# Optimization experiments

Measured on AMD Instinct MI355X. Metric: run time of the kernel, lower is better.

The kernel has to match this reference:

```python
import jax, jax.numpy as jnp
import numpy as np

N_NODES = 50000
N_EDGES = 1600000
NODE_DIM = 64
EDGE_DIM = 64
HID = 64
EPS = 1e-5


def _linear(x, W, b):
    return x @ W + b


def _layernorm(x, g, b):
    m = jnp.mean(x, axis=-1, keepdims=True)
    v = jnp.mean((x - m) ** 2, axis=-1, keepdims=True)
    return (x - m) * jax.lax.rsqrt(v + EPS) * g + b


def _mlp(x, p, pre):
    # Linear-ReLU, Linear-ReLU, Linear-LayerNorm
    h = jax.nn.relu(_linear(x, p[pre + 'W1'], p[pre + 'b1']))
    h = jax.nn.relu(_linear(h, p[pre + 'W2'], p[pre + 'b2']))
    h = _linear(h, p[pre + 'W3'], p[pre + 'b3'])
    return _layernorm(h, p[pre + 'g'], p[pre + 'beta'])


def setup_inputs() -> dict:
    key = jax.random.key(0)
    ks = jax.random.split(key, 16)
    inp = {
        'node_feat': jax.random.normal(ks[0], (N_NODES, NODE_DIM), jnp.float32),
        'edge_feat': jax.random.normal(ks[1], (N_EDGES, EDGE_DIM), jnp.float32),
        'edge_idx': jax.random.randint(ks[2], (N_EDGES, 2), 0, N_NODES, jnp.int32),
        'node_size': N_NODES,
    }
    s = 0.05
    e_in = EDGE_DIM + 2 * NODE_DIM
    n_in = NODE_DIM + EDGE_DIM
    inp['eW1'] = jax.random.normal(ks[3], (e_in, HID), jnp.float32) * s
    inp['eb1'] = jnp.zeros((HID,), jnp.float32)
    inp['eW2'] = jax.random.normal(ks[4], (HID, HID), jnp.float32) * s
    inp['eb2'] = jnp.zeros((HID,), jnp.float32)
    inp['eW3'] = jax.random.normal(ks[5], (HID, HID), jnp.float32) * s
    inp['eb3'] = jnp.zeros((HID,), jnp.float32)
    inp['eg'] = jnp.ones((HID,), jnp.float32)
    inp['ebeta'] = jnp.zeros((HID,), jnp.float32)
    inp['nW1'] = jax.random.normal(ks[6], (n_in, HID), jnp.float32) * s
    inp['nb1'] = jnp.zeros((HID,), jnp.float32)
    inp['nW2'] = jax.random.normal(ks[7], (HID, HID), jnp.float32) * s
    inp['nb2'] = jnp.zeros((HID,), jnp.float32)
    inp['nW3'] = jax.random.normal(ks[8], (HID, HID), jnp.float32) * s
    inp['nb3'] = jnp.zeros((HID,), jnp.float32)
    inp['ng'] = jnp.ones((HID,), jnp.float32)
    inp['nbeta'] = jnp.zeros((HID,), jnp.float32)
    return inp


def reference(node_feat, edge_feat, edge_idx, node_size,
              eW1, eb1, eW2, eb2, eW3, eb3, eg, ebeta,
              nW1, nb1, nW2, nb2, nW3, nb3, ng, nbeta):
    p = dict(eW1=eW1, eb1=eb1, eW2=eW2, eb2=eb2, eW3=eW3, eb3=eb3, eg=eg, ebeta=ebeta,
             nW1=nW1, nb1=nb1, nW2=nW2, nb2=nb2, nW3=nW3, nb3=nb3, ng=ng, nbeta=nbeta)
    center = edge_idx[:, 0]
    source = edge_idx[:, 1]
    # [E, edge_dim + 2*node_dim]
    stacked = jnp.concatenate([edge_feat, node_feat[center], node_feat[source]], axis=1)
    proc_edge_feat = _mlp(stacked, p, 'e')  # [E, 64]
    # scatter-add aggregate to nodes
    nodal_edge_feat = jax.ops.segment_sum(proc_edge_feat, center, num_segments=node_size)
    stacked_node = jnp.concatenate([node_feat, nodal_edge_feat], axis=1)  # [N, node_dim+64]
    proc_node_feat = _mlp(stacked_node, p, 'n')  # [N, 64]
    return proc_edge_feat, proc_node_feat
```

## Files before the change

kernel.cpp:

```cpp
#include <hip/hip_runtime.h>

typedef unsigned short u16;
typedef unsigned int u32;
typedef __attribute__((ext_vector_type(8))) __bf16 bf16x8;
typedef __attribute__((ext_vector_type(4))) float f32x4;
typedef __attribute__((ext_vector_type(2))) u32 u32x2;
typedef __attribute__((ext_vector_type(4))) u32 u32x4;

__device__ __forceinline__ u16 f2bf(float f) {
    u32 u = __float_as_uint(f);
    u = (u + 0x7FFFu + ((u >> 16) & 1u)) >> 16;
    return (u16)u;
}

__device__ __forceinline__ bf16x8 load8f_bf(const float* p) {
    f32x4 f0 = *(const f32x4*)p;
    f32x4 f1 = *(const f32x4*)(p + 4);
    bf16x8 r;
    r[0] = (__bf16)f0[0]; r[1] = (__bf16)f0[1]; r[2] = (__bf16)f0[2]; r[3] = (__bf16)f0[3];
    r[4] = (__bf16)f1[0]; r[5] = (__bf16)f1[1]; r[6] = (__bf16)f1[2]; r[7] = (__bf16)f1[3];
    return r;
}
__device__ __forceinline__ bf16x8 cvt2bf(f32x4 lo, f32x4 hi) {
    bf16x8 r;
    r[0] = (__bf16)lo[0]; r[1] = (__bf16)lo[1]; r[2] = (__bf16)lo[2]; r[3] = (__bf16)lo[3];
    r[4] = (__bf16)hi[0]; r[5] = (__bf16)hi[1]; r[6] = (__bf16)hi[2]; r[7] = (__bf16)hi[3];
    return r;
}
__device__ __forceinline__ u32 pk2(float x, float y) {
    __bf16 bx = (__bf16)x, by = (__bf16)y;
    return (u32)__builtin_bit_cast(u16, bx) | ((u32)__builtin_bit_cast(u16, by) << 16);
}

#define PK_EW1 0
#define PK_EW2 12288
#define PK_EW3 16384
#define PK_NW1 20480
#define PK_NW2 28672
#define PK_NW3 32768
#define PK_TOTAL 36864

__global__ void pack_weights_kernel(const float* __restrict__ eW1, const float* __restrict__ eW2,
                                    const float* __restrict__ eW3, const float* __restrict__ nW1,
                                    const float* __restrict__ nW2, const float* __restrict__ nW3,
                                    u16* __restrict__ P) {
    int idx = blockIdx.x * blockDim.x + threadIdx.x;
    if (idx >= PK_TOTAL) return;
    const float* W; int base;
    if (idx < PK_EW2)      { W = eW1; base = PK_EW1; }
    else if (idx < PK_EW3) { W = eW2; base = PK_EW2; }
    else if (idx < PK_NW1) { W = eW3; base = PK_EW3; }
    else if (idx < PK_NW2) { W = nW1; base = PK_NW1; }
    else if (idx < PK_NW3) { W = nW2; base = PK_NW2; }
    else                   { W = nW3; base = PK_NW3; }
    int r = idx - base;
    int j = r & 7, lane = (r >> 3) & 63, m = (r >> 9) & 3, s = r >> 11;
    int k = s * 32 + (lane >> 4) * 8 + j;
    int col = 16 * m + (lane & 15);
    P[idx] = f2bf(W[k * 64 + col]);
}

__global__ void degree_kernel(const int* __restrict__ edge_idx, int* __restrict__ deg, int E) {
    int e = blockIdx.x * blockDim.x + threadIdx.x;
    if (e < E) atomicAdd(&deg[edge_idx[2 * e]], 1);
}

__global__ void scan_blocks_kernel(const int* __restrict__ deg, int* __restrict__ off,
                                   int* __restrict__ partials, int N) {
    __shared__ int sh[256];
    const int t = threadIdx.x;
    const int g = blockIdx.x * 256 + t;
    int v = (g < N) ? deg[g] : 0;
    sh[t] = v;
    __syncthreads();
#pragma unroll
    for (int d = 1; d < 256; d <<= 1) {
        int add = (t >= d) ? sh[t - d] : 0;
        __syncthreads();
        sh[t] += add;
        __syncthreads();
    }
    if (g < N) off[g] = sh[t] - v;
    if (t == 255) partials[blockIdx.x] = sh[255];
}

__global__ void scan_partials_kernel(int* __restrict__ partials, int nparts) {
    __shared__ int sh[256];
    const int t = threadIdx.x;
    int v = (t < nparts) ? partials[t] : 0;
    sh[t] = v;
    __syncthreads();
#pragma unroll
    for (int d = 1; d < 256; d <<= 1) {
        int add = (t >= d) ? sh[t - d] : 0;
        __syncthreads();
        sh[t] += add;
        __syncthreads();
    }
    if (t < nparts) partials[t] = sh[t] - v;
}

__global__ void finalize_offsets_kernel(int* __restrict__ off, int* __restrict__ pos,
                                        const int* __restrict__ partials, int N, int E) {
    int g = blockIdx.x * blockDim.x + threadIdx.x;
    if (g < N) {
        int o = off[g] + partials[g >> 8];
        off[g] = o;
        pos[g] = o;
    }
    if (g == 0) off[N] = E;
}

__global__ void fill_csr_kernel(const int* __restrict__ edge_idx, int* __restrict__ pos,
                                int* __restrict__ csr, int E) {
    int e = blockIdx.x * blockDim.x + threadIdx.x;
    if (e < E) {
        int slot = atomicAdd(&pos[edge_idx[2 * e]], 1);
        csr[slot] = e;
    }
}

#define ET 2
__global__ __launch_bounds__(256) void edge_mlp_kernel(
    const float* __restrict__ node_feat, const float* __restrict__ edge_feat,
    const int* __restrict__ edge_idx, const u16* __restrict__ Pw,
    const float* __restrict__ b1g, const float* __restrict__ b2g, const float* __restrict__ b3g,
    const float* __restrict__ gg, const float* __restrict__ betag,
    float* __restrict__ out_edge, int E)
{
    __shared__ float params[5][64];
    __shared__ u16 htile[4][1024];
    const int tid = threadIdx.x;
    if (tid < 64) {
        params[0][tid] = b1g[tid];
        params[1][tid] = b2g[tid];
        params[2][tid] = b3g[tid];
        params[3][tid] = gg[tid];
        params[4][tid] = betag[tid];
    }
    __syncthreads();
    const int wid = tid >> 6, lane = tid & 63;
    const int er = lane & 15, a = lane >> 4;
    const int ebase = (blockIdx.x * 4 + wid) * (16 * ET);
    if (ebase >= E) return;
    u16* ht = htile[wid];
    const int swz = (er & 7) << 4;

    int eidx[ET], cn[ET], sn[ET];
#pragma unroll
    for (int t = 0; t < ET; ++t) {
        int e = ebase + t * 16 + er;
        if (e > E - 1) e = E - 1;
        eidx[t] = e;
        int2 ii = *(const int2*)(edge_idx + 2 * e);
        cn[t] = ii.x; sn[t] = ii.y;
    }

    f32x4 acc[ET][4];
#pragma unroll
    for (int t = 0; t < ET; ++t)
#pragma unroll
        for (int m = 0; m < 4; ++m) acc[t][m] = 0.0f;

#pragma unroll
    for (int s = 0; s < 6; ++s) {
        bf16x8 af[4];
#pragma unroll
        for (int m = 0; m < 4; ++m)
            af[m] = *(const bf16x8*)(Pw + PK_EW1 + ((s * 4 + m) * 64 + lane) * 8);
        bf16x8 bf[ET];
#pragma unroll
        for (int t = 0; t < ET; ++t) {
            const float* src;
            if (s < 2)      src = edge_feat + (size_t)eidx[t] * 64 + s * 32 + a * 8;
            else if (s < 4) src = node_feat + (size_t)cn[t] * 64 + (s - 2) * 32 + a * 8;
            else            src = node_feat + (size_t)sn[t] * 64 + (s - 4) * 32 + a * 8;
            bf[t] = load8f_bf(src);
        }
#pragma unroll
        for (int t = 0; t < ET; ++t)
#pragma unroll
            for (int m = 0; m < 4; ++m)
                acc[t][m] = __builtin_amdgcn_mfma_f32_16x16x32_bf16(af[m], bf[t], acc[t][m], 0, 0, 0);
    }

#pragma unroll
    for (int t = 0; t < ET; ++t) {
#pragma unroll
        for (int m = 0; m < 4; ++m) {
            float v0 = fmaxf(acc[t][m][0] + params[0][16 * m + 4 * a + 0], 0.0f);
            float v1 = fmaxf(acc[t][m][1] + params[0][16 * m + 4 * a + 1], 0.0f);
            float v2 = fmaxf(acc[t][m][2] + params[0][16 * m + 4 * a + 2], 0.0f);
            float v3 = fmaxf(acc[t][m][3] + params[0][16 * m + 4 * a + 3], 0.0f);
            u32x2 pv; pv[0] = pk2(v0, v1); pv[1] = pk2(v2, v3);
            int boff = (er * 128 + (16 * m + 4 * a) * 2) ^ swz;
            *(u32x2*)((char*)ht + boff) = pv;
        }
        f32x4 a2[4];
#pragma unroll
        for (int m = 0; m < 4; ++m) a2[m] = 0.0f;
#pragma unroll
        for (int s = 0; s < 2; ++s) {
            bf16x8 af[4];
#pragma unroll
            for (int m = 0; m < 4; ++m)
                af[m] = *(const bf16x8*)(Pw + PK_EW2 + ((s * 4 + m) * 64 + lane) * 8);
            int boff = (er * 128 + s * 64 + a * 16) ^ swz;
            bf16x8 bf = *(const bf16x8*)((char*)ht + boff);
#pragma unroll
            for (int m = 0; m < 4; ++m)
                a2[m] = __builtin_amdgcn_mfma_f32_16x16x32_bf16(af[m], bf, a2[m], 0, 0, 0);
        }
#pragma unroll
        for (int m = 0; m < 4; ++m) {
            float v0 = fmaxf(a2[m][0] + params[1][16 * m + 4 * a + 0], 0.0f);
            float v1 = fmaxf(a2[m][1] + params[1][16 * m + 4 * a + 1], 0.0f);
            float v2 = fmaxf(a2[m][2] + params[1][16 * m + 4 * a + 2], 0.0f);
            float v3 = fmaxf(a2[m][3] + params[1][16 * m + 4 * a + 3], 0.0f);
            u32x2 pv; pv[0] = pk2(v0, v1); pv[1] = pk2(v2, v3);
            int boff = (er * 128 + (16 * m + 4 * a) * 2) ^ swz;
            *(u32x2*)((char*)ht + boff) = pv;
        }
        f32x4 a3[4];
#pragma unroll
        for (int m = 0; m < 4; ++m) a3[m] = 0.0f;
#pragma unroll
        for (int s = 0; s < 2; ++s) {
            bf16x8 af[4];
#pragma unroll
            for (int m = 0; m < 4; ++m)
                af[m] = *(const bf16x8*)(Pw + PK_EW3 + ((s * 4 + m) * 64 + lane) * 8);
            int boff = (er * 128 + s * 64 + a * 16) ^ swz;
            bf16x8 bf = *(const bf16x8*)((char*)ht + boff);
#pragma unroll
            for (int m = 0; m < 4; ++m)
                a3[m] = __builtin_amdgcn_mfma_f32_16x16x32_bf16(af[m], bf, a3[m], 0, 0, 0);
        }
        float vals[16], sum = 0.0f, ssq = 0.0f;
#pragma unroll
        for (int m = 0; m < 4; ++m)
#pragma unroll
            for (int r = 0; r < 4; ++r) {
                float v = a3[m][r] + params[2][16 * m + 4 * a + r];
                vals[4 * m + r] = v; sum += v; ssq += v * v;
            }
        sum += __shfl_xor(sum, 16, 64); sum += __shfl_xor(sum, 32, 64);
        ssq += __shfl_xor(ssq, 16, 64); ssq += __shfl_xor(ssq, 32, 64);
        const float mean = sum * 0.015625f;
        const float var = ssq * 0.015625f - mean * mean;
        const float inv = rsqrtf(var + 1e-5f);
        const int e = ebase + t * 16 + er;
        if (e < E) {
#pragma unroll
            for (int m = 0; m < 4; ++m) {
                f32x4 o;
#pragma unroll
                for (int r = 0; r < 4; ++r) {
                    int f = 16 * m + 4 * a + r;
                    o[r] = (vals[4 * m + r] - mean) * inv * params[3][f] + params[4][f];
                }
                *(f32x4*)(out_edge + (size_t)e * 64 + 16 * m + 4 * a) = o;
            }
        }
    }
}

__global__ __launch_bounds__(256) void node_mlp_kernel(
    const float* __restrict__ node_feat, const float* __restrict__ proc_edge,
    const int* __restrict__ off, const int* __restrict__ csr,
    const u16* __restrict__ Pw,
    const float* __restrict__ b1g, const float* __restrict__ b2g, const float* __restrict__ b3g,
    const float* __restrict__ gg, const float* __restrict__ betag,
    float* __restrict__ out_node, int N)
{
    __shared__ float params[5][64];
    __shared__ u16 htile[4][1024];
    const int tid = threadIdx.x;
    if (tid < 64) {
        params[0][tid] = b1g[tid];
        params[1][tid] = b2g[tid];
        params[2][tid] = b3g[tid];
        params[3][tid] = gg[tid];
        params[4][tid] = betag[tid];
    }
    __syncthreads();
    const int wid = tid >> 6, lane = tid & 63;
    const int er = lane & 15, a = lane >> 4;
    const int nbase = (blockIdx.x * 4 + wid) * 16;
    if (nbase >= N) return;
    const int n = nbase + er;
    u16* ht = htile[wid];
    const int swz = (er & 7) << 4;

    f32x4 g0a = 0.0f, g0b = 0.0f, g1a = 0.0f, g1b = 0.0f;
    {
        const int beg = off[n], end = off[n + 1];
        int j = beg;
        for (; j + 7 < end; j += 8) {
#pragma unroll
            for (int u = 0; u < 8; ++u) {
                const float* row = proc_edge + (size_t)csr[j + u] * 64;
                g0a += *(const f32x4*)(row + a * 8);
                g0b += *(const f32x4*)(row + a * 8 + 4);
                g1a += *(const f32x4*)(row + 32 + a * 8);
                g1b += *(const f32x4*)(row + 32 + a * 8 + 4);
            }
        }
        for (; j < end; ++j) {
            const float* row = proc_edge + (size_t)csr[j] * 64;
            g0a += *(const f32x4*)(row + a * 8);
            g0b += *(const f32x4*)(row + a * 8 + 4);
            g1a += *(const f32x4*)(row + 32 + a * 8);
            g1b += *(const f32x4*)(row + 32 + a * 8 + 4);
        }
    }

    f32x4 acc[4];
#pragma unroll
    for (int m = 0; m < 4; ++m) acc[m] = 0.0f;

#pragma unroll
    for (int s = 0; s < 4; ++s) {
        bf16x8 af[4];
#pragma unroll
        for (int m = 0; m < 4; ++m)
            af[m] = *(const bf16x8*)(Pw + PK_NW1 + ((s * 4 + m) * 64 + lane) * 8);
        bf16x8 bf;
        if (s < 2)       bf = load8f_bf(node_feat + (size_t)n * 64 + s * 32 + a * 8);
        else if (s == 2) bf = cvt2bf(g0a, g0b);
        else             bf = cvt2bf(g1a, g1b);
#pragma unroll
        for (int m = 0; m < 4; ++m)
            acc[m] = __builtin_amdgcn_mfma_f32_16x16x32_bf16(af[m], bf, acc[m], 0, 0, 0);
    }
#pragma unroll
    for (int m = 0; m < 4; ++m) {
        float v0 = fmaxf(acc[m][0] + params[0][16 * m + 4 * a + 0], 0.0f);
        float v1 = fmaxf(acc[m][1] + params[0][16 * m + 4 * a + 1], 0.0f);
        float v2 = fmaxf(acc[m][2] + params[0][16 * m + 4 * a + 2], 0.0f);
        float v3 = fmaxf(acc[m][3] + params[0][16 * m + 4 * a + 3], 0.0f);
        u32x2 pv; pv[0] = pk2(v0, v1); pv[1] = pk2(v2, v3);
        int boff = (er * 128 + (16 * m + 4 * a) * 2) ^ swz;
        *(u32x2*)((char*)ht + boff) = pv;
    }

#pragma unroll
    for (int m = 0; m < 4; ++m) acc[m] = 0.0f;
#pragma unroll
    for (int s = 0; s < 2; ++s) {
        bf16x8 af[4];
#pragma unroll
        for (int m = 0; m < 4; ++m)
            af[m] = *(const bf16x8*)(Pw + PK_NW2 + ((s * 4 + m) * 64 + lane) * 8);
        int boff = (er * 128 + s * 64 + a * 16) ^ swz;
        bf16x8 bf = *(const bf16x8*)((char*)ht + boff);
#pragma unroll
        for (int m = 0; m < 4; ++m)
            acc[m] = __builtin_amdgcn_mfma_f32_16x16x32_bf16(af[m], bf, acc[m], 0, 0, 0);
    }
#pragma unroll
    for (int m = 0; m < 4; ++m) {
        float v0 = fmaxf(acc[m][0] + params[1][16 * m + 4 * a + 0], 0.0f);
        float v1 = fmaxf(acc[m][1] + params[1][16 * m + 4 * a + 1], 0.0f);
        float v2 = fmaxf(acc[m][2] + params[1][16 * m + 4 * a + 2], 0.0f);
        float v3 = fmaxf(acc[m][3] + params[1][16 * m + 4 * a + 3], 0.0f);
        u32x2 pv; pv[0] = pk2(v0, v1); pv[1] = pk2(v2, v3);
        int boff = (er * 128 + (16 * m + 4 * a) * 2) ^ swz;
        *(u32x2*)((char*)ht + boff) = pv;
    }

#pragma unroll
    for (int m = 0; m < 4; ++m) acc[m] = 0.0f;
#pragma unroll
    for (int s = 0; s < 2; ++s) {
        bf16x8 af[4];
#pragma unroll
        for (int m = 0; m < 4; ++m)
            af[m] = *(const bf16x8*)(Pw + PK_NW3 + ((s * 4 + m) * 64 + lane) * 8);
        int boff = (er * 128 + s * 64 + a * 16) ^ swz;
        bf16x8 bf = *(const bf16x8*)((char*)ht + boff);
#pragma unroll
        for (int m = 0; m < 4; ++m)
            acc[m] = __builtin_amdgcn_mfma_f32_16x16x32_bf16(af[m], bf, acc[m], 0, 0, 0);
    }
    float vals[16], sum = 0.0f, ssq = 0.0f;
#pragma unroll
    for (int m = 0; m < 4; ++m)
#pragma unroll
        for (int r = 0; r < 4; ++r) {
            float v = acc[m][r] + params[2][16 * m + 4 * a + r];
            vals[4 * m + r] = v; sum += v; ssq += v * v;
        }
    sum += __shfl_xor(sum, 16, 64); sum += __shfl_xor(sum, 32, 64);
    ssq += __shfl_xor(ssq, 16, 64); ssq += __shfl_xor(ssq, 32, 64);
    const float mean = sum * 0.015625f;
    const float var = ssq * 0.015625f - mean * mean;
    const float inv = rsqrtf(var + 1e-5f);
#pragma unroll
    for (int m = 0; m < 4; ++m) {
        f32x4 o;
#pragma unroll
        for (int r = 0; r < 4; ++r) {
            int f = 16 * m + 4 * a + r;
            o[r] = (vals[4 * m + r] - mean) * inv * params[3][f] + params[4][f];
        }
        *(f32x4*)(out_node + (size_t)n * 64 + 16 * m + 4 * a) = o;
    }
}

extern "C" void kernel_launch(void* const* d_in, const int* in_sizes, int n_in,
                              void* d_out, int out_size, void* d_ws, size_t ws_size,
                              hipStream_t stream) {
    const float* node_feat = (const float*)d_in[0];
    const float* edge_feat = (const float*)d_in[1];
    const int* edge_idx  = (const int*)d_in[2];
    const float* eW1 = (const float*)d_in[4];
    const float* eb1 = (const float*)d_in[5];
    const float* eW2 = (const float*)d_in[6];
    const float* eb2 = (const float*)d_in[7];
    const float* eW3 = (const float*)d_in[8];
    const float* eb3 = (const float*)d_in[9];
    const float* eg  = (const float*)d_in[10];
    const float* ebt = (const float*)d_in[11];
    const float* nW1 = (const float*)d_in[12];
    const float* nb1 = (const float*)d_in[13];
    const float* nW2 = (const float*)d_in[14];
    const float* nb2 = (const float*)d_in[15];
    const float* nW3 = (const float*)d_in[16];
    const float* nb3 = (const float*)d_in[17];
    const float* ng  = (const float*)d_in[18];
    const float* nbt = (const float*)d_in[19];

    const int N = in_sizes[0] / 64;
    const int E = in_sizes[1] / 64;
    const int nparts = (N + 255) / 256;

    char* w = (char*)d_ws;
    int* off      = (int*)w;                    w += (size_t)(N + 1) * 4;
    int* pos      = (int*)w;                    w += (size_t)N * 4;
    int* partials = (int*)w;                    w += 256 * 4;
    int* csr      = (int*)w;                    w += (size_t)E * 4;
    u16* Pw       = (u16*)w;

    float* out_edge = (float*)d_out;
    float* out_node = out_edge + (size_t)E * 64;

    pack_weights_kernel<<<(PK_TOTAL + 255) / 256, 256, 0, stream>>>(eW1, eW2, eW3, nW1, nW2, nW3, Pw);

    const int eblocks = (E + (64 * ET) - 1) / (64 * ET);
    edge_mlp_kernel<<<eblocks, 256, 0, stream>>>(node_feat, edge_feat, edge_idx, Pw,
                                                 eb1, eb2, eb3, eg, ebt, out_edge, E);

    hipMemsetAsync(pos, 0, (size_t)N * 4, stream);
    degree_kernel<<<(E + 255) / 256, 256, 0, stream>>>(edge_idx, pos, E);
    scan_blocks_kernel<<<nparts, 256, 0, stream>>>(pos, off, partials, N);
    scan_partials_kernel<<<1, 256, 0, stream>>>(partials, nparts);
    finalize_offsets_kernel<<<(N + 255) / 256, 256, 0, stream>>>(off, pos, partials, N, E);
    fill_csr_kernel<<<(E + 255) / 256, 256, 0, stream>>>(edge_idx, pos, csr, E);

    const int nblocks = (N + 63) / 64;
    node_mlp_kernel<<<nblocks, 256, 0, stream>>>(node_feat, out_edge, off, csr, Pw,
                                                 nb1, nb2, nb3, ng, nbt, out_node, N);
}
```

Baseline: 648.1 us.

## Stage edge weights in LDS and split node aggregation into wave-per-node gather

```diff
diff --git a/kernel.cpp b/kernel.cpp
--- a/kernel.cpp
+++ b/kernel.cpp
@@ -12,20 +12,14 @@
     u = (u + 0x7FFFu + ((u >> 16) & 1u)) >> 16;
     return (u16)u;
 }
-
-__device__ __forceinline__ bf16x8 load8f_bf(const float* p) {
-    f32x4 f0 = *(const f32x4*)p;
-    f32x4 f1 = *(const f32x4*)(p + 4);
-    bf16x8 r;
-    r[0] = (__bf16)f0[0]; r[1] = (__bf16)f0[1]; r[2] = (__bf16)f0[2]; r[3] = (__bf16)f0[3];
-    r[4] = (__bf16)f1[0]; r[5] = (__bf16)f1[1]; r[6] = (__bf16)f1[2]; r[7] = (__bf16)f1[3];
-    return r;
-}
 __device__ __forceinline__ bf16x8 cvt2bf(f32x4 lo, f32x4 hi) {
     bf16x8 r;
     r[0] = (__bf16)lo[0]; r[1] = (__bf16)lo[1]; r[2] = (__bf16)lo[2]; r[3] = (__bf16)lo[3];
     r[4] = (__bf16)hi[0]; r[5] = (__bf16)hi[1]; r[6] = (__bf16)hi[2]; r[7] = (__bf16)hi[3];
     return r;
+}
+__device__ __forceinline__ bf16x8 load8f_bf(const float* p) {
+    return cvt2bf(*(const f32x4*)p, *(const f32x4*)(p + 4));
 }
 __device__ __forceinline__ u32 pk2(float x, float y) {
     __bf16 bx = (__bf16)x, by = (__bf16)y;
@@ -39,6 +33,7 @@
 #define PK_NW2 28672
 #define PK_NW3 32768
 #define PK_TOTAL 36864
+#define EW_U16 20480
 
 __global__ void pack_weights_kernel(const float* __restrict__ eW1, const float* __restrict__ eW2,
                                     const float* __restrict__ eW3, const float* __restrict__ nW1,
@@ -120,6 +115,39 @@
     }
 }
 
+__global__ __launch_bounds__(256) void gather_kernel(
+    const float* __restrict__ proc_edge, const int* __restrict__ off,
+    const int* __restrict__ csr, u16* __restrict__ nodal16, int N)
+{
+    const int wid = threadIdx.x >> 6, lane = threadIdx.x & 63;
+    const int n = blockIdx.x * 4 + wid;
+    if (n >= N) return;
+    const int r = lane >> 4;
+    const int q = lane & 15;
+    const int beg = off[n], end = off[n + 1];
+    f32x4 v0 = 0.0f, v1 = 0.0f;
+    int j = beg + r;
+    for (; j + 4 < end; j += 8) {
+        int e0 = csr[j], e1 = csr[j + 4];
+        v0 += *(const f32x4*)(proc_edge + (size_t)e0 * 64 + q * 4);
+        v1 += *(const f32x4*)(proc_edge + (size_t)e1 * 64 + q * 4);
+    }
+    if (j < end) {
+        int e0 = csr[j];
+        v0 += *(const f32x4*)(proc_edge + (size_t)e0 * 64 + q * 4);
+    }
+    v0 += v1;
+#pragma unroll
+    for (int i = 0; i < 4; ++i) {
+        v0[i] += __shfl_xor(v0[i], 16, 64);
+        v0[i] += __shfl_xor(v0[i], 32, 64);
+    }
+    if (r == 0) {
+        u32x2 pv; pv[0] = pk2(v0[0], v0[1]); pv[1] = pk2(v0[2], v0[3]);
+        *(u32x2*)(nodal16 + (size_t)n * 64 + q * 4) = pv;
+    }
+}
+
 #define ET 2
 __global__ __launch_bounds__(256) void edge_mlp_kernel(
     const float* __restrict__ node_feat, const float* __restrict__ edge_feat,
@@ -128,9 +156,15 @@
     const float* __restrict__ gg, const float* __restrict__ betag,
     float* __restrict__ out_edge, int E)
 {
+    __shared__ u16 wlds[EW_U16];
+    __shared__ u16 htile[4][1024];
     __shared__ float params[5][64];
-    __shared__ u16 htile[4][1024];
     const int tid = threadIdx.x;
+#pragma unroll
+    for (int i = 0; i < 10; ++i) {
+        u32x4 v = *(const u32x4*)(Pw + (size_t)(i * 256 + tid) * 8);
+        *(u32x4*)(wlds + (size_t)(i * 256 + tid) * 8) = v;
+    }
     if (tid < 64) {
         params[0][tid] = b1g[tid];
         params[1][tid] = b2g[tid];
@@ -139,6 +173,7 @@
         params[4][tid] = betag[tid];
     }
     __syncthreads();
+
     const int wid = tid >> 6, lane = tid & 63;
     const int er = lane & 15, a = lane >> 4;
     const int ebase = (blockIdx.x * 4 + wid) * (16 * ET);
@@ -163,25 +198,26 @@
         for (int m = 0; m < 4; ++m) acc[t][m] = 0.0f;
 
 #pragma unroll
-    for (int s = 0; s < 6; ++s) {
-        bf16x8 af[4];
-#pragma unroll
-        for (int m = 0; m < 4; ++m)
-            af[m] = *(const bf16x8*)(Pw + PK_EW1 + ((s * 4 + m) * 64 + lane) * 8);
-        bf16x8 bf[ET];
-#pragma unroll
-        for (int t = 0; t < ET; ++t) {
+    for (int t = 0; t < ET; ++t) {
+        f32x4 raw[12];
+#pragma unroll
+        for (int s = 0; s < 6; ++s) {
             const float* src;
             if (s < 2)      src = edge_feat + (size_t)eidx[t] * 64 + s * 32 + a * 8;
             else if (s < 4) src = node_feat + (size_t)cn[t] * 64 + (s - 2) * 32 + a * 8;
             else            src = node_feat + (size_t)sn[t] * 64 + (s - 4) * 32 + a * 8;
-            bf[t] = load8f_bf(src);
-        }
-#pragma unroll
-        for (int t = 0; t < ET; ++t)
-#pragma unroll
-            for (int m = 0; m < 4; ++m)
-                acc[t][m] = __builtin_amdgcn_mfma_f32_16x16x32_bf16(af[m], bf[t], acc[t][m], 0, 0, 0);
+            raw[2 * s]     = *(const f32x4*)src;
+            raw[2 * s + 1] = *(const f32x4*)(src + 4);
+        }
+#pragma unroll
+        for (int s = 0; s < 6; ++s) {
+            bf16x8 bf = cvt2bf(raw[2 * s], raw[2 * s + 1]);
+#pragma unroll
+            for (int m = 0; m < 4; ++m) {
+                bf16x8 af = *(const bf16x8*)(wlds + PK_EW1 + ((s * 4 + m) * 64 + lane) * 8);
+                acc[t][m] = __builtin_amdgcn_mfma_f32_16x16x32_bf16(af, bf, acc[t][m], 0, 0, 0);
+            }
+        }
     }
 
 #pragma unroll
@@ -201,15 +237,13 @@
         for (int m = 0; m < 4; ++m) a2[m] = 0.0f;
 #pragma unroll
         for (int s = 0; s < 2; ++s) {
-            bf16x8 af[4];
-#pragma unroll
-            for (int m = 0; m < 4; ++m)
-                af[m] = *(const bf16x8*)(Pw + PK_EW2 + ((s * 4 + m) * 64 + lane) * 8);
             int boff = (er * 128 + s * 64 + a * 16) ^ swz;
             bf16x8 bf = *(const bf16x8*)((char*)ht + boff);
 #pragma unroll
-            for (int m = 0; m < 4; ++m)
-                a2[m] = __builtin_amdgcn_mfma_f32_16x16x32_bf16(af[m], bf, a2[m], 0, 0, 0);
+            for (int m = 0; m < 4; ++m) {
+                bf16x8 af = *(const bf16x8*)(wlds + PK_EW2 + ((s * 4 + m) * 64 + lane) * 8);
+                a2[m] = __builtin_amdgcn_mfma_f32_16x16x32_bf16(af, bf, a2[m], 0, 0, 0);
+            }
         }
 #pragma unroll
         for (int m = 0; m < 4; ++m) {
@@ -226,15 +260,13 @@
         for (int m = 0; m < 4; ++m) a3[m] = 0.0f;
 #pragma unroll
         for (int s = 0; s < 2; ++s) {
-            bf16x8 af[4];
-#pragma unroll
-            for (int m = 0; m < 4; ++m)
-                af[m] = *(const bf16x8*)(Pw + PK_EW3 + ((s * 4 + m) * 64 + lane) * 8);
             int boff = (er * 128 + s * 64 + a * 16) ^ swz;
             bf16x8 bf = *(const bf16x8*)((char*)ht + boff);
 #pragma unroll
-            for (int m = 0; m < 4; ++m)
-                a3[m] = __builtin_amdgcn_mfma_f32_16x16x32_bf16(af[m], bf, a3[m], 0, 0, 0);
+            for (int m = 0; m < 4; ++m) {
+                bf16x8 af = *(const bf16x8*)(wlds + PK_EW3 + ((s * 4 + m) * 64 + lane) * 8);
+                a3[m] = __builtin_amdgcn_mfma_f32_16x16x32_bf16(af, bf, a3[m], 0, 0, 0);
+            }
         }
         float vals[16], sum = 0.0f, ssq = 0.0f;
 #pragma unroll
@@ -266,8 +298,7 @@
 }
 
 __global__ __launch_bounds__(256) void node_mlp_kernel(
-    const float* __restrict__ node_feat, const float* __restrict__ proc_edge,
-    const int* __restrict__ off, const int* __restrict__ csr,
+    const float* __restrict__ node_feat, const u16* __restrict__ nodal16,
     const u16* __restrict__ Pw,
     const float* __restrict__ b1g, const float* __restrict__ b2g, const float* __restrict__ b3g,
     const float* __restrict__ gg, const float* __restrict__ betag,
@@ -292,29 +323,6 @@
     u16* ht = htile[wid];
     const int swz = (er & 7) << 4;
 
-    f32x4 g0a = 0.0f, g0b = 0.0f, g1a = 0.0f, g1b = 0.0f;
-    {
-        const int beg = off[n], end = off[n + 1];
-        int j = beg;
-        for (; j + 7 < end; j += 8) {
-#pragma unroll
-            for (int u = 0; u < 8; ++u) {
-                const float* row = proc_edge + (size_t)csr[j + u] * 64;
-                g0a += *(const f32x4*)(row + a * 8);
-                g0b += *(const f32x4*)(row + a * 8 + 4);
-                g1a += *(const f32x4*)(row + 32 + a * 8);
-                g1b += *(const f32x4*)(row + 32 + a * 8 + 4);
-            }
-        }
-        for (; j < end; ++j) {
-            const float* row = proc_edge + (size_t)csr[j] * 64;
-            g0a += *(const f32x4*)(row + a * 8);
-            g0b += *(const f32x4*)(row + a * 8 + 4);
-            g1a += *(const f32x4*)(row + 32 + a * 8);
-            g1b += *(const f32x4*)(row + 32 + a * 8 + 4);
-        }
-    }
-
     f32x4 acc[4];
 #pragma unroll
     for (int m = 0; m < 4; ++m) acc[m] = 0.0f;
@@ -326,9 +334,8 @@
         for (int m = 0; m < 4; ++m)
             af[m] = *(const bf16x8*)(Pw + PK_NW1 + ((s * 4 + m) * 64 + lane) * 8);
         bf16x8 bf;
-        if (s < 2)       bf = load8f_bf(node_feat + (size_t)n * 64 + s * 32 + a * 8);
-        else if (s == 2) bf = cvt2bf(g0a, g0b);
-        else             bf = cvt2bf(g1a, g1b);
+        if (s < 2) bf = load8f_bf(node_feat + (size_t)n * 64 + s * 32 + a * 8);
+        else       bf = *(const bf16x8*)(nodal16 + (size_t)n * 64 + (s - 2) * 32 + a * 8);
 #pragma unroll
         for (int m = 0; m < 4; ++m)
             acc[m] = __builtin_amdgcn_mfma_f32_16x16x32_bf16(af[m], bf, acc[m], 0, 0, 0);
@@ -440,7 +447,8 @@
     int* pos      = (int*)w;                    w += (size_t)N * 4;
     int* partials = (int*)w;                    w += 256 * 4;
     int* csr      = (int*)w;                    w += (size_t)E * 4;
-    u16* Pw       = (u16*)w;
+    u16* Pw       = (u16*)w;                    w += (size_t)PK_TOTAL * 2;
+    u16* nodal16  = (u16*)w;
 
     float* out_edge = (float*)d_out;
     float* out_node = out_edge + (size_t)E * 64;
@@ -458,7 +466,9 @@
     finalize_offsets_kernel<<<(N + 255) / 256, 256, 0, stream>>>(off, pos, partials, N, E);
     fill_csr_kernel<<<(E + 255) / 256, 256, 0, stream>>>(edge_idx, pos, csr, E);
 
+    gather_kernel<<<(N + 3) / 4, 256, 0, stream>>>(out_edge, off, csr, nodal16, N);
+
     const int nblocks = (N + 63) / 64;
-    node_mlp_kernel<<<nblocks, 256, 0, stream>>>(node_feat, out_edge, off, csr, Pw,
+    node_mlp_kernel<<<nblocks, 256, 0, stream>>>(node_feat, nodal16, Pw,
                                                  nb1, nb2, nb3, ng, nbt, out_node, N);
 }
```

Result: faster. 580.3 us (-10.5%).
